# Kernel tuning notes

Hardware: AMD Instinct MI355X
Metric: run time of the kernel (lower is better)

Reference implementation:

```python
import jax, jax.numpy as jnp
import numpy as np

N_AGENTS = 262144
GRID = 1024
C = 8
HIDDEN = 64
DT = 0.1
SENSOR_ANGLE = 0.6
SENSOR_LEN = 3.0
DECAY = 0.99


def setup_inputs() -> dict:
    key = jax.random.key(0)
    k1, k2, k3, k4, k5 = jax.random.split(key, 5)
    agent_pos = jax.random.uniform(k1, (2, N_AGENTS), minval=2.0, maxval=GRID - 2.0, dtype=jnp.float32)
    agent_vel = jax.random.uniform(k2, (2, N_AGENTS), minval=-1.0, maxval=1.0, dtype=jnp.float32)
    pheremone_lattice = jax.random.uniform(k3, (C, GRID, GRID), dtype=jnp.float32)
    W1 = jax.random.normal(k4, (3 * C, HIDDEN), dtype=jnp.float32) * 0.1
    b1 = jnp.zeros((HIDDEN,), dtype=jnp.float32)
    W2 = jax.random.normal(k5, (HIDDEN, 2 + C), dtype=jnp.float32) * 0.1
    b2 = jnp.zeros((2 + C,), dtype=jnp.float32)
    return {"agent_pos": agent_pos, "agent_vel": agent_vel, "pheremone_lattice": pheremone_lattice,
            "W1": W1, "b1": b1, "W2": W2, "b2": b2}


def _sense(agent_pos, agent_vel, lattice):
    # heading angle per agent, 3 sensor offsets: 0, +a, -a
    theta = jnp.arctan2(agent_vel[1], agent_vel[0])                      # [N]
    offs = jnp.array([0.0, SENSOR_ANGLE, -SENSOR_ANGLE], dtype=agent_pos.dtype)
    ang = theta[None, :] + offs[:, None]                                  # [3,N]
    cx = jnp.rint(agent_pos[0][None, :] + SENSOR_LEN * jnp.cos(ang)).astype(jnp.int32)  # [3,N]
    cy = jnp.rint(agent_pos[1][None, :] + SENSOR_LEN * jnp.sin(ang)).astype(jnp.int32)
    d = jnp.array([-1, 0, 1], dtype=jnp.int32)
    xi = (cx[:, :, None] + d) % GRID                                      # [3,N,3]
    yi = (cy[:, :, None] + d) % GRID
    # Cartesian product of x and y offsets (meshgrid in original) -> 3x3 window
    X = xi[:, :, :, None]                                                 # [3,N,3,1]
    Y = yi[:, :, None, :]                                                 # [3,N,1,3]
    vals = lattice[:, X, Y]                                               # [C,3,N,3,3]
    w = vals.sum(axis=(-1, -2))                                           # [C,3,N]
    return w[:, 0].T, w[:, 1].T, w[:, 2].T                                # each [N,C]


def reference(agent_pos, agent_vel, pheremone_lattice, W1, b1, W2, b2):
    w_front, w_left, w_right = _sense(agent_pos, agent_vel, pheremone_lattice)
    # per-agent MLP (vmapped agent_nn in original): concat 3 sensor readings
    x = jnp.concatenate([w_front, w_left, w_right], axis=-1)              # [N,3C]
    h = jnp.tanh(x @ W1 + b1)                                             # [N,HIDDEN]
    o = h @ W2 + b2                                                       # [N,2+C]
    new_vel = o[:, :2].T                                                  # [2,N]
    d_pher = o[:, 2:].T                                                   # [C,N]
    # deposit pheremones at rounded agent positions (scatter-set, relu clamp)
    pos_i = jnp.rint(agent_pos).astype(jnp.int32)                         # [2,N]
    cur = pheremone_lattice[:, pos_i[0], pos_i[1]]                        # [C,N]
    lat = pheremone_lattice.at[:, pos_i[0], pos_i[1]].set(jax.nn.relu(cur + DT * d_pher))
    # gaussian_blur == 0 -> diffusion is identity; then decay
    lat = lat * DECAY
    # periodic position update
    new_pos = (agent_pos + new_vel * DT) % GRID
    return (new_pos, new_vel, lat)
```

## Files before the change

### kernel.cpp

```cpp
#include <hip/hip_runtime.h>
#include <hip/hip_bf16.h>
#include <math.h>

#define GRIDN 1024
#define NAGENTS 262144
#define CCH 8
#define HIDDEN 64
#define DT 0.1f
#define DECAYF 0.99f
#define SENSOR_LEN 3.0f
#define COS_SA 0.82533561490967829724f
#define SIN_SA 0.56464247339503535720f

typedef __attribute__((ext_vector_type(8))) short short8;

__device__ __forceinline__ float fast_tanh(float x) {
    float xc = fminf(fmaxf(x, -9.0f), 9.0f);
    float t = __builtin_amdgcn_exp2f(xc * 2.88539008177792681472f);
    return (t - 1.0f) * __builtin_amdgcn_rcpf(t + 1.0f);
}

__device__ __forceinline__ float bf16_lo(unsigned u) {
    return __builtin_bit_cast(float, u << 16);
}
__device__ __forceinline__ float bf16_hi(unsigned u) {
    return __builtin_bit_cast(float, u & 0xffff0000u);
}

__global__ void __launch_bounds__(256) k_boxT(const float* __restrict__ lat,
                                              __hip_bfloat16* __restrict__ BT,
                                              int* __restrict__ winner) {
    int idx = blockIdx.x * blockDim.x + threadIdx.x;
    winner[idx] = -1;
    int x = idx >> 10, y = idx & (GRIDN - 1);
    int xm = (x + GRIDN - 1) & (GRIDN - 1), xp = (x + 1) & (GRIDN - 1);
    int ym = (y + GRIDN - 1) & (GRIDN - 1), yp = (y + 1) & (GRIDN - 1);
    __hip_bfloat16 out[CCH];
#pragma unroll
    for (int c = 0; c < CCH; ++c) {
        const float* L = lat + (size_t)c * GRIDN * GRIDN;
        const float* r0 = L + xm * GRIDN;
        const float* r1 = L + x * GRIDN;
        const float* r2 = L + xp * GRIDN;
        float s = r0[ym] + r0[y] + r0[yp]
                + r1[ym] + r1[y] + r1[yp]
                + r2[ym] + r2[y] + r2[yp];
        out[c] = __float2bfloat16(s);
    }
    *(short8*)(BT + (size_t)idx * CCH) = *(const short8*)out;
}

__global__ void __launch_bounds__(256) k_agent(
    const float* __restrict__ pos, const float* __restrict__ vel,
    const __hip_bfloat16* __restrict__ BT,
    const float* __restrict__ W1, const float* __restrict__ b1,
    const float* __restrict__ W2, const float* __restrict__ b2,
    float* __restrict__ out_pos, float* __restrict__ out_vel,
    float* __restrict__ dp, int* __restrict__ winner) {
    __shared__ float part[4][64][13];

    int lane = threadIdx.x & 63;
    int wq = __builtin_amdgcn_readfirstlane(threadIdx.x >> 6);
    int i = blockIdx.x * 64 + lane;

    float px = pos[i], py = pos[i + NAGENTS];
    float vx = vel[i], vy = vel[i + NAGENTS];

    float r2 = vx * vx + vy * vy;
    float ct, st;
    if (r2 > 0.f) {
        float inv = rsqrtf(r2);
        ct = vx * inv;
        st = vy * inv;
    } else {
        ct = 1.f;
        st = 0.f;
    }

    float dirx[3], diry[3];
    dirx[0] = ct;                          diry[0] = st;
    dirx[1] = ct * COS_SA - st * SIN_SA;   diry[1] = st * COS_SA + ct * SIN_SA;
    dirx[2] = ct * COS_SA + st * SIN_SA;   diry[2] = st * COS_SA - ct * SIN_SA;

    uint4 raw[3];
#pragma unroll
    for (int s = 0; s < 3; ++s) {
        int gx = ((int)rintf(px + SENSOR_LEN * dirx[s]) + GRIDN) & (GRIDN - 1);
        int gy = ((int)rintf(py + SENSOR_LEN * diry[s]) + GRIDN) & (GRIDN - 1);
        raw[s] = *(const uint4*)(BT + ((size_t)(gx << 10) + gy) * CCH);
    }
    unsigned xk[12];
#pragma unroll
    for (int s = 0; s < 3; ++s) {
        xk[s * 4 + 0] = raw[s].x; xk[s * 4 + 1] = raw[s].y;
        xk[s * 4 + 2] = raw[s].z; xk[s * 4 + 3] = raw[s].w;
    }

    float h[16];
    {
        const float4* b1v = (const float4*)(b1 + wq * 16);
#pragma unroll
        for (int q = 0; q < 4; ++q) {
            float4 b = b1v[q];
            h[q * 4 + 0] = b.x; h[q * 4 + 1] = b.y;
            h[q * 4 + 2] = b.z; h[q * 4 + 3] = b.w;
        }
    }
#pragma unroll
    for (int k = 0; k < 3 * CCH; ++k) {
        float xv = (k & 1) ? bf16_hi(xk[k >> 1]) : bf16_lo(xk[k >> 1]);
        const float4* wr = (const float4*)(W1 + k * HIDDEN + wq * 16);
#pragma unroll
        for (int q = 0; q < 4; ++q) {
            float4 w = wr[q];
            h[q * 4 + 0] = fmaf(xv, w.x, h[q * 4 + 0]);
            h[q * 4 + 1] = fmaf(xv, w.y, h[q * 4 + 1]);
            h[q * 4 + 2] = fmaf(xv, w.z, h[q * 4 + 2]);
            h[q * 4 + 3] = fmaf(xv, w.w, h[q * 4 + 3]);
        }
    }

    float o[2 + CCH];
#pragma unroll
    for (int k = 0; k < 2 + CCH; ++k) o[k] = 0.f;
#pragma unroll
    for (int jj = 0; jj < 16; ++jj) {
        float tj = fast_tanh(h[jj]);
        const float* w2 = W2 + (wq * 16 + jj) * (2 + CCH);
#pragma unroll
        for (int k = 0; k < 2 + CCH; ++k) o[k] = fmaf(tj, w2[k], o[k]);
    }

#pragma unroll
    for (int k = 0; k < 2 + CCH; ++k) part[wq][lane][k] = o[k];
    __syncthreads();

    if (wq == 0) {
        float s0 = part[0][lane][0] + part[1][lane][0] + part[2][lane][0] + part[3][lane][0] + b2[0];
        float s1 = part[0][lane][1] + part[1][lane][1] + part[2][lane][1] + part[3][lane][1] + b2[1];
        float npx = px + s0 * DT;
        if (npx >= (float)GRIDN) npx -= (float)GRIDN;
        if (npx < 0.f) npx += (float)GRIDN;
        float npy = py + s1 * DT;
        if (npy >= (float)GRIDN) npy -= (float)GRIDN;
        if (npy < 0.f) npy += (float)GRIDN;
        out_pos[i] = npx;
        out_pos[i + NAGENTS] = npy;
        out_vel[i] = s0;
        out_vel[i + NAGENTS] = s1;
    } else if (wq == 1) {
        float d0 = part[0][lane][2] + part[1][lane][2] + part[2][lane][2] + part[3][lane][2] + b2[2];
        float d1 = part[0][lane][3] + part[1][lane][3] + part[2][lane][3] + part[3][lane][3] + b2[3];
        float d2 = part[0][lane][4] + part[1][lane][4] + part[2][lane][4] + part[3][lane][4] + b2[4];
        float d3 = part[0][lane][5] + part[1][lane][5] + part[2][lane][5] + part[3][lane][5] + b2[5];
        *(float4*)(dp + (size_t)i * CCH) = make_float4(d0, d1, d2, d3);
    } else if (wq == 2) {
        float d4 = part[0][lane][6] + part[1][lane][6] + part[2][lane][6] + part[3][lane][6] + b2[6];
        float d5 = part[0][lane][7] + part[1][lane][7] + part[2][lane][7] + part[3][lane][7] + b2[7];
        float d6 = part[0][lane][8] + part[1][lane][8] + part[2][lane][8] + part[3][lane][8] + b2[8];
        float d7 = part[0][lane][9] + part[1][lane][9] + part[2][lane][9] + part[3][lane][9] + b2[9];
        *(float4*)(dp + (size_t)i * CCH + 4) = make_float4(d4, d5, d6, d7);
    } else {
        int wx = (int)rintf(px) & (GRIDN - 1);
        int wy = (int)rintf(py) & (GRIDN - 1);
        atomicMax(&winner[(wx << 10) + wy], i);
    }
}

__global__ void __launch_bounds__(256) k_update(const float* __restrict__ lat,
                                                const int* __restrict__ winner,
                                                const float* __restrict__ dp,
                                                float* __restrict__ out_lat) {
    int idx = blockIdx.x * blockDim.x + threadIdx.x;
    int w = winner[idx];
    float d[CCH];
    if (w >= 0) {
        const float4* dpp = (const float4*)(dp + (size_t)w * CCH);
        float4 a = dpp[0], b = dpp[1];
        d[0] = a.x; d[1] = a.y; d[2] = a.z; d[3] = a.w;
        d[4] = b.x; d[5] = b.y; d[6] = b.z; d[7] = b.w;
    }
#pragma unroll
    for (int c = 0; c < CCH; ++c) {
        size_t off = (size_t)c * GRIDN * GRIDN + idx;
        float v = lat[off];
        if (w >= 0) v = fmaxf(v + DT * d[c], 0.f);
        out_lat[off] = v * DECAYF;
    }
}

extern "C" void kernel_launch(void* const* d_in, const int* in_sizes, int n_in,
                              void* d_out, int out_size, void* d_ws, size_t ws_size,
                              hipStream_t stream) {
    const float* pos = (const float*)d_in[0];
    const float* vel = (const float*)d_in[1];
    const float* lat = (const float*)d_in[2];
    const float* W1  = (const float*)d_in[3];
    const float* b1  = (const float*)d_in[4];
    const float* W2  = (const float*)d_in[5];
    const float* b2  = (const float*)d_in[6];

    float* out      = (float*)d_out;
    float* out_pos  = out;
    float* out_vel  = out + 2 * NAGENTS;
    float* out_lat  = out + 4 * NAGENTS;

    char* ws = (char*)d_ws;
    int*            winner = (int*)ws;
    float*          dp     = (float*)(ws + (4 << 20));
    __hip_bfloat16* BT     = (__hip_bfloat16*)(ws + (12 << 20));

    const int ncell = GRIDN * GRIDN;

    k_boxT<<<ncell / 256, 256, 0, stream>>>(lat, BT, winner);
    k_agent<<<NAGENTS / 64, 256, 0, stream>>>(pos, vel, BT, W1, b1, W2, b2,
                                              out_pos, out_vel, dp, winner);
    k_update<<<ncell / 256, 256, 0, stream>>>(lat, winner, dp, out_lat);
}
```

Measured before the change: 62.07 us.

## Switch agent MLP to packed fp16 dot2 with pre-packed weights

Stores the box-summed lattice as fp16 instead of bf16, packs W1 and W2 into fp16 pairs in the first block of the box kernel, and computes both MLP layers with v_dot2 fp16 instructions. This halves the FMA instruction count and the weight loads in the agent kernel. The cost is lower precision: fp16 has a narrower range for box sums, and tanh outputs are rounded to fp16. The weight packing adds a serial prologue to one block of the box kernel.

```diff
diff --git a/kernel.cpp b/kernel.cpp
--- a/kernel.cpp
+++ b/kernel.cpp
@@ -13,6 +13,24 @@
 #define SIN_SA 0.56464247339503535720f
 
 typedef __attribute__((ext_vector_type(8))) short short8;
+typedef __attribute__((ext_vector_type(2))) _Float16 half2v;
+
+__device__ __forceinline__ float dot2f(unsigned a, unsigned b, float c) {
+#if __has_builtin(__builtin_amdgcn_fdot2)
+    return __builtin_amdgcn_fdot2(__builtin_bit_cast(half2v, a),
+                                  __builtin_bit_cast(half2v, b), c, false);
+#else
+    half2v ha = __builtin_bit_cast(half2v, a), hb = __builtin_bit_cast(half2v, b);
+    return c + (float)ha.x * (float)hb.x + (float)ha.y * (float)hb.y;
+#endif
+}
+
+__device__ __forceinline__ unsigned packh(float a, float b) {
+    _Float16 ha = (_Float16)a, hb = (_Float16)b;
+    unsigned short ua = __builtin_bit_cast(unsigned short, ha);
+    unsigned short ub = __builtin_bit_cast(unsigned short, hb);
+    return (unsigned)ua | ((unsigned)ub << 16);
+}
 
 __device__ __forceinline__ float fast_tanh(float x) {
     float xc = fminf(fmaxf(x, -9.0f), 9.0f);
@@ -20,22 +38,33 @@
     return (t - 1.0f) * __builtin_amdgcn_rcpf(t + 1.0f);
 }
 
-__device__ __forceinline__ float bf16_lo(unsigned u) {
-    return __builtin_bit_cast(float, u << 16);
-}
-__device__ __forceinline__ float bf16_hi(unsigned u) {
-    return __builtin_bit_cast(float, u & 0xffff0000u);
-}
-
 __global__ void __launch_bounds__(256) k_boxT(const float* __restrict__ lat,
-                                              __hip_bfloat16* __restrict__ BT,
-                                              int* __restrict__ winner) {
+                                              _Float16* __restrict__ BT,
+                                              int* __restrict__ winner,
+                                              const float* __restrict__ W1,
+                                              const float* __restrict__ W2,
+                                              unsigned* __restrict__ W1p,
+                                              unsigned* __restrict__ W2p) {
+    if (blockIdx.x == 0) {
+        for (int t = threadIdx.x; t < 768 + 512; t += 256) {
+            if (t < 768) {
+                int p = t >> 6, j = t & 63;
+                W1p[t] = packh(W1[(2 * p) * HIDDEN + j], W1[(2 * p + 1) * HIDDEN + j]);
+            } else {
+                int q = t - 768;
+                int pg = q >> 4, k = q & 15;
+                unsigned v = 0;
+                if (k < 10) v = packh(W2[(2 * pg) * 10 + k], W2[(2 * pg + 1) * 10 + k]);
+                W2p[q] = v;
+            }
+        }
+    }
     int idx = blockIdx.x * blockDim.x + threadIdx.x;
     winner[idx] = -1;
     int x = idx >> 10, y = idx & (GRIDN - 1);
     int xm = (x + GRIDN - 1) & (GRIDN - 1), xp = (x + 1) & (GRIDN - 1);
     int ym = (y + GRIDN - 1) & (GRIDN - 1), yp = (y + 1) & (GRIDN - 1);
-    __hip_bfloat16 out[CCH];
+    _Float16 out[CCH];
 #pragma unroll
     for (int c = 0; c < CCH; ++c) {
         const float* L = lat + (size_t)c * GRIDN * GRIDN;
@@ -45,16 +74,16 @@
         float s = r0[ym] + r0[y] + r0[yp]
                 + r1[ym] + r1[y] + r1[yp]
                 + r2[ym] + r2[y] + r2[yp];
-        out[c] = __float2bfloat16(s);
+        out[c] = (_Float16)s;
     }
     *(short8*)(BT + (size_t)idx * CCH) = *(const short8*)out;
 }
 
 __global__ void __launch_bounds__(256) k_agent(
     const float* __restrict__ pos, const float* __restrict__ vel,
-    const __hip_bfloat16* __restrict__ BT,
-    const float* __restrict__ W1, const float* __restrict__ b1,
-    const float* __restrict__ W2, const float* __restrict__ b2,
+    const _Float16* __restrict__ BT,
+    const unsigned* __restrict__ W1p, const float* __restrict__ b1,
+    const unsigned* __restrict__ W2p, const float* __restrict__ b2,
     float* __restrict__ out_pos, float* __restrict__ out_vel,
     float* __restrict__ dp, int* __restrict__ winner) {
     __shared__ float part[4][64][13];
@@ -107,28 +136,26 @@
         }
     }
 #pragma unroll
-    for (int k = 0; k < 3 * CCH; ++k) {
-        float xv = (k & 1) ? bf16_hi(xk[k >> 1]) : bf16_lo(xk[k >> 1]);
-        const float4* wr = (const float4*)(W1 + k * HIDDEN + wq * 16);
-#pragma unroll
-        for (int q = 0; q < 4; ++q) {
-            float4 w = wr[q];
-            h[q * 4 + 0] = fmaf(xv, w.x, h[q * 4 + 0]);
-            h[q * 4 + 1] = fmaf(xv, w.y, h[q * 4 + 1]);
-            h[q * 4 + 2] = fmaf(xv, w.z, h[q * 4 + 2]);
-            h[q * 4 + 3] = fmaf(xv, w.w, h[q * 4 + 3]);
-        }
-    }
+    for (int p = 0; p < 12; ++p) {
+        unsigned xp = xk[p];
+        const unsigned* wrow = W1p + p * HIDDEN + wq * 16;
+#pragma unroll
+        for (int jj = 0; jj < 16; ++jj) h[jj] = dot2f(xp, wrow[jj], h[jj]);
+    }
+
+    unsigned hp[8];
+#pragma unroll
+    for (int p = 0; p < 8; ++p)
+        hp[p] = packh(fast_tanh(h[2 * p]), fast_tanh(h[2 * p + 1]));
 
     float o[2 + CCH];
 #pragma unroll
     for (int k = 0; k < 2 + CCH; ++k) o[k] = 0.f;
 #pragma unroll
-    for (int jj = 0; jj < 16; ++jj) {
-        float tj = fast_tanh(h[jj]);
-        const float* w2 = W2 + (wq * 16 + jj) * (2 + CCH);
-#pragma unroll
-        for (int k = 0; k < 2 + CCH; ++k) o[k] = fmaf(tj, w2[k], o[k]);
+    for (int p = 0; p < 8; ++p) {
+        const unsigned* w2row = W2p + (wq * 8 + p) * 16;
+#pragma unroll
+        for (int k = 0; k < 2 + CCH; ++k) o[k] = dot2f(hp[p], w2row[k], o[k]);
     }
 
 #pragma unroll
@@ -206,14 +233,16 @@
     float* out_lat  = out + 4 * NAGENTS;
 
     char* ws = (char*)d_ws;
-    int*            winner = (int*)ws;
-    float*          dp     = (float*)(ws + (4 << 20));
-    __hip_bfloat16* BT     = (__hip_bfloat16*)(ws + (12 << 20));
+    int*       winner = (int*)ws;
+    float*     dp     = (float*)(ws + (4 << 20));
+    _Float16*  BT     = (_Float16*)(ws + (12 << 20));
+    unsigned*  W1p    = (unsigned*)(ws + (28 << 20));
+    unsigned*  W2p    = (unsigned*)(ws + (28 << 20) + 4096);
 
     const int ncell = GRIDN * GRIDN;
 
-    k_boxT<<<ncell / 256, 256, 0, stream>>>(lat, BT, winner);
-    k_agent<<<NAGENTS / 64, 256, 0, stream>>>(pos, vel, BT, W1, b1, W2, b2,
+    k_boxT<<<ncell / 256, 256, 0, stream>>>(lat, BT, winner, W1, W2, W1p, W2p);
+    k_agent<<<NAGENTS / 64, 256, 0, stream>>>(pos, vel, BT, W1p, b1, W2p, b2,
                                               out_pos, out_vel, dp, winner);
     k_update<<<ncell / 256, 256, 0, stream>>>(lat, winner, dp, out_lat);
 }
```

After: 60.59 us. -2.4%, faster.
